# Optimization experiments

Measured on AMD Instinct MI355X. Metric: run time of the kernel, lower is better.

The kernel has to match this reference:

```python
import jax, jax.numpy as jnp
import numpy as np

NUM_SEQS = 4
SEQ_LEN = 2048
T = NUM_SEQS * SEQ_LEN          # total tokens
D_IN = 4096
D_OUT = 4096
NUM_ADAPTERS = 8
MAX_RANK = 64
CACHE_LEN = NUM_ADAPTERS * MAX_RANK  # 512 pages


def setup_inputs() -> dict:
    key = jax.random.key(0)
    ks = jax.random.split(key, 8)
    x = jax.random.normal(ks[0], (T, D_IN), dtype=jnp.float32)
    weight = jax.random.normal(ks[1], (D_OUT, D_IN), dtype=jnp.float32) * 0.02
    bias = jax.random.normal(ks[2], (D_OUT,), dtype=jnp.float32) * 0.02
    a_cache = jax.random.normal(ks[3], (CACHE_LEN, D_IN), dtype=jnp.float32) * 0.02
    b_cache = jax.random.normal(ks[4], (CACHE_LEN, D_OUT), dtype=jnp.float32) * 0.02
    b_start_loc = (jnp.arange(NUM_SEQS) * SEQ_LEN).astype(jnp.int32)
    b_adapter_ids = jax.random.randint(ks[5], (NUM_SEQS,), 0, NUM_ADAPTERS).astype(jnp.int32)
    b_scaling = jax.random.uniform(ks[6], (NUM_SEQS,), dtype=jnp.float32, minval=0.5, maxval=2.0)
    # page i for (adapter a, rank slot r) lives at a*MAX_RANK + r
    rank_page_table = jnp.arange(CACHE_LEN, dtype=jnp.int32).reshape(NUM_ADAPTERS, MAX_RANK)
    ranks = jax.random.randint(ks[7], (NUM_ADAPTERS,), 1, MAX_RANK + 1).astype(jnp.int32)
    return {"x": x, "weight": weight, "bias": bias, "a_cache": a_cache,
            "b_cache": b_cache, "b_start_loc": b_start_loc,
            "b_adapter_ids": b_adapter_ids, "b_scaling": b_scaling,
            "rank_page_table": rank_page_table, "ranks": ranks}


def reference(x, weight, bias, a_cache, b_cache, b_start_loc,
              b_adapter_ids, b_scaling, rank_page_table, ranks):
    t = x.shape[0]
    num_adapters, max_rank = rank_page_table.shape
    # map each token to its sequence -> adapter id / scaling (mbgmm dispatch)
    seg = jnp.searchsorted(b_start_loc, jnp.arange(t, dtype=b_start_loc.dtype),
                           side='right') - 1                      # [T]
    tok_adapter = b_adapter_ids[seg]                              # [T]
    tok_scale = b_scaling[seg]                                    # [T]
    # gather paged LoRA A/B weights per adapter: [A, R, D]
    A_all = a_cache[rank_page_table]                              # [A, R, D_in]
    B_all = b_cache[rank_page_table]                              # [A, R, D_out]
    # mbgmm_a: xa[t, r] = x[t] . A[adapter(t), r], zero beyond rank
    xa_all = jnp.einsum('td,ard->tar', x, A_all)                  # [T, A, R]
    rmask = (jnp.arange(max_rank)[None, :] < ranks[:, None])      # [A, R]
    onehot = (tok_adapter[:, None] == jnp.arange(num_adapters)[None, :])  # [T, A]
    sel = (onehot[:, :, None] & rmask[None, :, :]).astype(x.dtype)  # [T, A, R]
    xa_sel = xa_all * sel
    # mbgmm_b: lora_out[t] = scaling * sum_r xa[t, r] * B[adapter(t), r]
    lora_out = jnp.einsum('tar,aro->to', xa_sel, B_all) * tok_scale[:, None]
    base_out = x @ weight.T + bias
    return base_out + lora_out
```

## Files before the change

kernel.cpp:

```cpp
#include <hip/hip_runtime.h>
#include <hip/hip_bf16.h>

typedef unsigned short u16;
typedef unsigned int u32;
typedef __attribute__((ext_vector_type(8))) short bf16x8;
typedef __attribute__((ext_vector_type(4))) float f32x4;

#define T_TOK 8192
#define DIN 4096
#define DOUT 4096
#define N_SEQS 4
#define N_ADPT 8
#define MAXR 64
#define CACHE_LEN 512

__device__ __forceinline__ u16 f2bf(float f) {
    u32 u = __builtin_bit_cast(u32, f);
    u += 0x7fffu + ((u >> 16) & 1u);
    return (u16)(u >> 16);
}

__device__ __forceinline__ void load_lds16(const u16* g, u16* l) {
    __builtin_amdgcn_global_load_lds(
        (const __attribute__((address_space(1))) u32*)g,
        (__attribute__((address_space(3))) u32*)l, 16, 0, 0);
}

__global__ void cvt_kernel(const float* __restrict__ in, u16* __restrict__ out, int n4) {
    int i = blockIdx.x * blockDim.x + threadIdx.x;
    int stride = gridDim.x * blockDim.x;
    for (; i < n4; i += stride) {
        float4 v = reinterpret_cast<const float4*>(in)[i];
        ushort4 o;
        o.x = f2bf(v.x); o.y = f2bf(v.y); o.z = f2bf(v.z); o.w = f2bf(v.w);
        reinterpret_cast<ushort4*>(out)[i] = o;
    }
}

__global__ void build_bt(const float* __restrict__ b_cache, const int* __restrict__ rpt,
                         u16* __restrict__ Bt) {
    int id = blockIdx.x * 256 + threadIdx.x;
    int n  = id & (DOUT - 1);
    int rb = (id >> 12) & 7;
    int a  = id >> 15;
    union { u16 u[8]; uint4 v; } pack;
    #pragma unroll
    for (int j = 0; j < 8; ++j) {
        int r = rb * 8 + j;
        int page = rpt[a * MAXR + r];
        pack.u[j] = f2bf(b_cache[(long)page * DOUT + n]);
    }
    *reinterpret_cast<uint4*>(&Bt[((long)(a * DOUT + n)) * MAXR + rb * 8]) = pack.v;
}

__launch_bounds__(256)
__global__ void xa_kernel(const u16* __restrict__ xb, const u16* __restrict__ ab,
                          const int* __restrict__ b_start_loc,
                          const int* __restrict__ b_adapter_ids,
                          const float* __restrict__ b_scaling,
                          const int* __restrict__ rpt,
                          const int* __restrict__ ranks,
                          u16* __restrict__ xa) {
    int t0 = blockIdx.x * 128;
    int seg = 0;
    #pragma unroll
    for (int i = 1; i < N_SEQS; ++i) if (b_start_loc[i] <= t0) seg = i;
    int adapter = b_adapter_ids[seg];
    float scale = b_scaling[seg];
    int rank = ranks[adapter];

    __shared__ __attribute__((aligned(16))) u16 As[128 * 32];
    __shared__ __attribute__((aligned(16))) u16 Bs[64 * 32];

    int tid = threadIdx.x;
    int lane = tid & 63, wave = tid >> 6;
    int lr = lane & 15, lk = lane >> 4;

    int e0 = wave * 64 + lane;
    int e1 = 256 + e0;
    int ra0 = e0 >> 2, ca0 = (e0 & 3) * 8;
    int ra1 = e1 >> 2, ca1 = (e1 & 3) * 8;
    const u16* gA0 = xb + (long)(t0 + ra0) * DIN + ca0;
    const u16* gA1 = xb + (long)(t0 + ra1) * DIN + ca1;
    int rB = ra0;
    int page = rpt[adapter * MAXR + rB];
    const u16* gB = ab + (long)page * DIN + ca0;

    f32x4 acc[2][4] = {};

    for (int k0 = 0; k0 < DIN; k0 += 32) {
        load_lds16(gA0 + k0, As + wave * 512);
        load_lds16(gA1 + k0, As + 2048 + wave * 512);
        load_lds16(gB + k0,  Bs + wave * 512);
        asm volatile("s_waitcnt vmcnt(0)" ::: "memory");
        __syncthreads();
        bf16x8 af[2], bfr[4];
        #pragma unroll
        for (int m = 0; m < 2; ++m)
            af[m] = *(const bf16x8*)&As[(wave * 32 + m * 16 + lr) * 32 + lk * 8];
        #pragma unroll
        for (int n = 0; n < 4; ++n)
            bfr[n] = *(const bf16x8*)&Bs[(n * 16 + lr) * 32 + lk * 8];
        #pragma unroll
        for (int m = 0; m < 2; ++m)
            #pragma unroll
            for (int n = 0; n < 4; ++n)
                acc[m][n] = __builtin_amdgcn_mfma_f32_16x16x32_bf16(af[m], bfr[n], acc[m][n], 0, 0, 0);
        __syncthreads();
    }

    #pragma unroll
    for (int m = 0; m < 2; ++m) {
        int trow = t0 + wave * 32 + m * 16 + lk * 4;
        #pragma unroll
        for (int n = 0; n < 4; ++n) {
            int r = n * 16 + lr;
            #pragma unroll
            for (int j = 0; j < 4; ++j) {
                float v = (r < rank) ? acc[m][n][j] * scale : 0.0f;
                xa[(long)(trow + j) * MAXR + r] = f2bf(v);
            }
        }
    }
}

__launch_bounds__(512, 2)
__global__ void gemm256_kernel(const u16* __restrict__ xb, const u16* __restrict__ wb,
                               const float* __restrict__ bias,
                               const u16* __restrict__ xa, const u16* __restrict__ Bt,
                               const int* __restrict__ b_start_loc,
                               const int* __restrict__ b_adapter_ids,
                               float* __restrict__ out) {
    __shared__ __attribute__((aligned(16))) u16 lds[32768];

    int bid = blockIdx.x;
    int wgid = (bid & 7) * 64 + (bid >> 3);
    int mt = wgid >> 4, nt = wgid & 15;
    int brow = mt * 256, bcol = nt * 256;

    int seg = 0;
    #pragma unroll
    for (int i = 1; i < N_SEQS; ++i) if (b_start_loc[i] <= brow) seg = i;
    int adapter = b_adapter_ids[seg];

    int tid = threadIdx.x;
    int lane = tid & 63, wave = tid >> 6;
    int wm = wave >> 2, wn = wave & 3;
    int lr = lane & 15, lk = lane >> 4;

    int lsw = (tid & 7) ^ ((tid >> 3) & 7);
    int c8  = (lsw & 3) * 8;
    int r0  = (tid >> 3) * 2 + (lsw >> 2);
    const long odA0 = (long)(brow + r0) * DIN + c8;
    const long odA1 = odA0 + 128L * DIN;
    const long odB0 = (long)(bcol + r0) * DIN + c8;
    const long odB1 = odB0 + 128L * DIN;
    const long o6A0 = (long)(brow + r0) * MAXR + c8;
    const long o6A1 = o6A0 + 128L * MAXR;
    const long o6B0 = (long)(adapter * DOUT + bcol + r0) * MAXR + c8;
    const long o6B1 = o6B0 + 128L * MAXR;

    #define STAGE(T, buf)                                                          \
        do {                                                                       \
            u16* dA = lds + (buf) * 8192 + tid * 8;                                \
            u16* dB = lds + 16384 + (buf) * 8192 + tid * 8;                        \
            if ((T) < 128) {                                                       \
                long ko = (long)(T) * 32;                                          \
                load_lds16(xb + odA0 + ko, dA);                                    \
                load_lds16(xb + odA1 + ko, dA + 4096);                             \
                load_lds16(wb + odB0 + ko, dB);                                    \
                load_lds16(wb + odB1 + ko, dB + 4096);                             \
            } else {                                                               \
                long ko = (long)((T) - 128) * 32;                                  \
                load_lds16(xa + o6A0 + ko, dA);                                    \
                load_lds16(xa + o6A1 + ko, dA + 4096);                             \
                load_lds16(Bt + o6B0 + ko, dB);                                    \
                load_lds16(Bt + o6B1 + ko, dB + 4096);                             \
            }                                                                      \
        } while (0)

    const int laneByte = (lr >> 1) * 128 + 16 * ((((lr & 1) << 2) + lk) ^ (lr >> 1));
    const char* ldsc = (const char*)lds;
    const int cA = wm * 8192 + laneByte;
    const int cB = 32768 + wn * 4096 + laneByte;

    #define READF(FA, FB, par)                                                     \
        do {                                                                       \
            const char* pA = ldsc + (par) * 16384 + cA;                            \
            const char* pB = ldsc + (par) * 16384 + cB;                            \
            _Pragma("unroll")                                                      \
            for (int ni = 0; ni < 4; ++ni) FB[ni] = *(const bf16x8*)(pB + ni * 1024); \
            _Pragma("unroll")                                                      \
            for (int mi = 0; mi < 8; ++mi) FA[mi] = *(const bf16x8*)(pA + mi * 1024); \
        } while (0)

    #define MFMA32(FA, FB)                                                         \
        do {                                                                       \
            __builtin_amdgcn_s_setprio(1);                                         \
            _Pragma("unroll")                                                      \
            for (int mi = 0; mi < 8; ++mi)                                         \
                _Pragma("unroll")                                                  \
                for (int ni = 0; ni < 4; ++ni)                                     \
                    acc[mi][ni] = __builtin_amdgcn_mfma_f32_16x16x32_bf16(         \
                        FA[mi], FB[ni], acc[mi][ni], 0, 0, 0);                     \
            __builtin_amdgcn_s_setprio(0);                                         \
        } while (0)

    #define ENDBAR()                                                               \
        do {                                                                       \
            asm volatile("s_waitcnt lgkmcnt(0)" ::: "memory");                     \
            __builtin_amdgcn_sched_barrier(0);                                     \
            __builtin_amdgcn_s_barrier();                                          \
        } while (0)

    f32x4 acc[8][4] = {};
    bf16x8 fA0[8], fB0[4], fA1[8], fB1[4];

    STAGE(0, 0);
    STAGE(1, 1);
    asm volatile("s_waitcnt vmcnt(4)" ::: "memory");
    __builtin_amdgcn_s_barrier();
    READF(fA0, fB0, 0);
    ENDBAR();

    for (int t = 0; t < 130; t += 2) {
        STAGE((t + 2 < 130) ? t + 2 : 129, t & 1);
        asm volatile("s_waitcnt vmcnt(4)" ::: "memory");
        __builtin_amdgcn_s_barrier();
        READF(fA1, fB1, (t + 1) & 1);
        MFMA32(fA0, fB0);
        ENDBAR();

        STAGE((t + 3 < 130) ? t + 3 : 129, (t + 1) & 1);
        asm volatile("s_waitcnt vmcnt(4)" ::: "memory");
        __builtin_amdgcn_s_barrier();
        if (t + 2 < 130) READF(fA0, fB0, t & 1);
        MFMA32(fA1, fB1);
        ENDBAR();
    }
    asm volatile("s_waitcnt vmcnt(0)" ::: "memory");

    #undef STAGE
    #undef READF
    #undef MFMA32
    #undef ENDBAR

    #pragma unroll
    for (int m = 0; m < 8; ++m) {
        int orow = brow + wm * 128 + m * 16 + lk * 4;
        #pragma unroll
        for (int n = 0; n < 4; ++n) {
            int ocol = bcol + wn * 64 + n * 16 + lr;
            float bv = bias[ocol];
            #pragma unroll
            for (int j = 0; j < 4; ++j)
                out[(long)(orow + j) * DOUT + ocol] = acc[m][n][j] + bv;
        }
    }
}

extern "C" void kernel_launch(void* const* d_in, const int* in_sizes, int n_in,
                              void* d_out, int out_size, void* d_ws, size_t ws_size,
                              hipStream_t stream) {
    const float* x          = (const float*)d_in[0];
    const float* weight     = (const float*)d_in[1];
    const float* bias       = (const float*)d_in[2];
    const float* a_cache    = (const float*)d_in[3];
    const float* b_cache    = (const float*)d_in[4];
    const int*   b_start    = (const int*)d_in[5];
    const int*   b_adapter  = (const int*)d_in[6];
    const float* b_scaling  = (const float*)d_in[7];
    const int*   rpt        = (const int*)d_in[8];
    const int*   ranks      = (const int*)d_in[9];
    float* out = (float*)d_out;

    char* ws = (char*)d_ws;
    u16* xb = (u16*)ws; ws += (size_t)T_TOK * DIN * 2;
    u16* wb = (u16*)ws; ws += (size_t)DOUT * DIN * 2;
    u16* ab = (u16*)ws; ws += (size_t)CACHE_LEN * DIN * 2;
    u16* Bt = (u16*)ws; ws += (size_t)N_ADPT * DOUT * MAXR * 2;
    u16* xa = (u16*)ws; ws += (size_t)T_TOK * MAXR * 2;

    cvt_kernel<<<2048, 256, 0, stream>>>(x, xb, T_TOK * DIN / 4);
    cvt_kernel<<<2048, 256, 0, stream>>>(weight, wb, DOUT * DIN / 4);
    cvt_kernel<<<512, 256, 0, stream>>>(a_cache, ab, CACHE_LEN * DIN / 4);
    build_bt<<<(N_ADPT * 8 * DOUT) / 256, 256, 0, stream>>>(b_cache, rpt, Bt);
    xa_kernel<<<T_TOK / 128, 256, 0, stream>>>(xb, ab, b_start, b_adapter, b_scaling, rpt, ranks, xa);
    gemm256_kernel<<<(T_TOK / 256) * (DOUT / 256), 512, 0, stream>>>(xb, wb, bias, xa, Bt, b_start, b_adapter, out);
}
```

Baseline: 366.9 us.

## Use 32x32x16 MFMA in main GEMM and double-buffer xa kernel loads

The main GEMM now uses 32x32x16 bf16 MFMA instructions with a 4x2 grid of 16-wide accumulators instead of 8x4 16x16x32 tiles. The LDS fragment addressing and output-store indexing are rewritten to match the new operand layout. Fewer, larger MFMAs per k-step should raise matrix-core throughput and cut LDS reads per FLOP. Separately, the xa kernel gets double-buffered LDS with a prefetch of the next k-slice, overlapping global loads with compute. The risk is wrong swizzle or lane mapping and more register pressure.

```diff
diff --git a/kernel.cpp b/kernel.cpp
--- a/kernel.cpp
+++ b/kernel.cpp
@@ -5,6 +5,7 @@
 typedef unsigned int u32;
 typedef __attribute__((ext_vector_type(8))) short bf16x8;
 typedef __attribute__((ext_vector_type(4))) float f32x4;
+typedef __attribute__((ext_vector_type(16))) float f32x16;
 
 #define T_TOK 8192
 #define DIN 4096
@@ -69,8 +70,8 @@
     float scale = b_scaling[seg];
     int rank = ranks[adapter];
 
-    __shared__ __attribute__((aligned(16))) u16 As[128 * 32];
-    __shared__ __attribute__((aligned(16))) u16 Bs[64 * 32];
+    __shared__ __attribute__((aligned(16))) u16 As[2 * 4096];
+    __shared__ __attribute__((aligned(16))) u16 Bs[2 * 2048];
 
     int tid = threadIdx.x;
     int lane = tid & 63, wave = tid >> 6;
@@ -88,26 +89,42 @@
 
     f32x4 acc[2][4] = {};
 
-    for (int k0 = 0; k0 < DIN; k0 += 32) {
-        load_lds16(gA0 + k0, As + wave * 512);
-        load_lds16(gA1 + k0, As + 2048 + wave * 512);
-        load_lds16(gB + k0,  Bs + wave * 512);
-        asm volatile("s_waitcnt vmcnt(0)" ::: "memory");
-        __syncthreads();
+    #define XSTAGE(s, buf)                                                         \
+        do {                                                                       \
+            load_lds16(gA0 + (s) * 32, As + (buf) * 4096 + wave * 512);            \
+            load_lds16(gA1 + (s) * 32, As + (buf) * 4096 + 2048 + wave * 512);     \
+            load_lds16(gB + (s) * 32,  Bs + (buf) * 2048 + wave * 512);            \
+        } while (0)
+
+    XSTAGE(0, 0);
+    for (int s = 0; s < 128; ++s) {
+        int b = s & 1;
+        if (s < 127) {
+            XSTAGE(s + 1, b ^ 1);
+            asm volatile("s_waitcnt vmcnt(3)" ::: "memory");
+        } else {
+            asm volatile("s_waitcnt vmcnt(0)" ::: "memory");
+        }
+        __builtin_amdgcn_s_barrier();
+        __builtin_amdgcn_sched_barrier(0);
+
         bf16x8 af[2], bfr[4];
         #pragma unroll
         for (int m = 0; m < 2; ++m)
-            af[m] = *(const bf16x8*)&As[(wave * 32 + m * 16 + lr) * 32 + lk * 8];
+            af[m] = *(const bf16x8*)&As[b * 4096 + (wave * 32 + m * 16 + lr) * 32 + lk * 8];
         #pragma unroll
         for (int n = 0; n < 4; ++n)
-            bfr[n] = *(const bf16x8*)&Bs[(n * 16 + lr) * 32 + lk * 8];
+            bfr[n] = *(const bf16x8*)&Bs[b * 2048 + (n * 16 + lr) * 32 + lk * 8];
         #pragma unroll
         for (int m = 0; m < 2; ++m)
             #pragma unroll
             for (int n = 0; n < 4; ++n)
                 acc[m][n] = __builtin_amdgcn_mfma_f32_16x16x32_bf16(af[m], bfr[n], acc[m][n], 0, 0, 0);
-        __syncthreads();
-    }
+
+        __builtin_amdgcn_s_barrier();
+        __builtin_amdgcn_sched_barrier(0);
+    }
+    #undef XSTAGE
 
     #pragma unroll
     for (int m = 0; m < 2; ++m) {
@@ -146,7 +163,9 @@
     int tid = threadIdx.x;
     int lane = tid & 63, wave = tid >> 6;
     int wm = wave >> 2, wn = wave & 3;
+    int l5 = lane & 31, k8 = lane >> 5;
     int lr = lane & 15, lk = lane >> 4;
+    (void)lr; (void)lk;
 
     int lsw = (tid & 7) ^ ((tid >> 3) & 7);
     int c8  = (lsw & 3) * 8;
@@ -179,30 +198,38 @@
             }                                                                      \
         } while (0)
 
-    const int laneByte = (lr >> 1) * 128 + 16 * ((((lr & 1) << 2) + lk) ^ (lr >> 1));
+    const int lb0 = (l5 >> 1) * 128 + (((((l5 & 1) << 2) + 0 + k8) ^ ((l5 >> 1) & 7)) * 16);
+    const int lb1 = (l5 >> 1) * 128 + (((((l5 & 1) << 2) + 2 + k8) ^ ((l5 >> 1) & 7)) * 16);
     const char* ldsc = (const char*)lds;
-    const int cA = wm * 8192 + laneByte;
-    const int cB = 32768 + wn * 4096 + laneByte;
+    const int cA0 = wm * 8192 + lb0, cA1 = wm * 8192 + lb1;
+    const int cB0 = 32768 + wn * 4096 + lb0, cB1 = 32768 + wn * 4096 + lb1;
 
     #define READF(FA, FB, par)                                                     \
         do {                                                                       \
-            const char* pA = ldsc + (par) * 16384 + cA;                            \
-            const char* pB = ldsc + (par) * 16384 + cB;                            \
+            const char* pA0 = ldsc + (par) * 16384 + cA0;                          \
+            const char* pA1 = ldsc + (par) * 16384 + cA1;                          \
+            const char* pB0 = ldsc + (par) * 16384 + cB0;                          \
+            const char* pB1 = ldsc + (par) * 16384 + cB1;                          \
+            FB[0] = *(const bf16x8*)(pB0);        FB[1] = *(const bf16x8*)(pB0 + 2048); \
+            FB[2] = *(const bf16x8*)(pB1);        FB[3] = *(const bf16x8*)(pB1 + 2048); \
             _Pragma("unroll")                                                      \
-            for (int ni = 0; ni < 4; ++ni) FB[ni] = *(const bf16x8*)(pB + ni * 1024); \
-            _Pragma("unroll")                                                      \
-            for (int mi = 0; mi < 8; ++mi) FA[mi] = *(const bf16x8*)(pA + mi * 1024); \
-        } while (0)
-
-    #define MFMA32(FA, FB)                                                         \
+            for (int mi = 0; mi < 4; ++mi) {                                       \
+                FA[mi]     = *(const bf16x8*)(pA0 + mi * 2048);                    \
+                FA[4 + mi] = *(const bf16x8*)(pA1 + mi * 2048);                    \
+            }                                                                      \
+        } while (0)
+
+    #define MFMA16(FA, FB)                                                         \
         do {                                                                       \
             __builtin_amdgcn_s_setprio(1);                                         \
             _Pragma("unroll")                                                      \
-            for (int mi = 0; mi < 8; ++mi)                                         \
+            for (int ks = 0; ks < 2; ++ks)                                         \
                 _Pragma("unroll")                                                  \
-                for (int ni = 0; ni < 4; ++ni)                                     \
-                    acc[mi][ni] = __builtin_amdgcn_mfma_f32_16x16x32_bf16(         \
-                        FA[mi], FB[ni], acc[mi][ni], 0, 0, 0);                     \
+                for (int mi = 0; mi < 4; ++mi)                                     \
+                    _Pragma("unroll")                                              \
+                    for (int ni = 0; ni < 2; ++ni)                                 \
+                        acc[mi][ni] = __builtin_amdgcn_mfma_f32_32x32x16_bf16(     \
+                            FA[ks * 4 + mi], FB[ks * 2 + ni], acc[mi][ni], 0, 0, 0); \
             __builtin_amdgcn_s_setprio(0);                                         \
         } while (0)
 
@@ -213,7 +240,7 @@
             __builtin_amdgcn_s_barrier();                                          \
         } while (0)
 
-    f32x4 acc[8][4] = {};
+    f32x16 acc[4][2] = {};
     bf16x8 fA0[8], fB0[4], fA1[8], fB1[4];
 
     STAGE(0, 0);
@@ -228,33 +255,36 @@
         asm volatile("s_waitcnt vmcnt(4)" ::: "memory");
         __builtin_amdgcn_s_barrier();
         READF(fA1, fB1, (t + 1) & 1);
-        MFMA32(fA0, fB0);
+        MFMA16(fA0, fB0);
         ENDBAR();
 
         STAGE((t + 3 < 130) ? t + 3 : 129, (t + 1) & 1);
         asm volatile("s_waitcnt vmcnt(4)" ::: "memory");
         __builtin_amdgcn_s_barrier();
         if (t + 2 < 130) READF(fA0, fB0, t & 1);
-        MFMA32(fA1, fB1);
+        MFMA16(fA1, fB1);
         ENDBAR();
     }
     asm volatile("s_waitcnt vmcnt(0)" ::: "memory");
 
     #undef STAGE
     #undef READF
-    #undef MFMA32
+    #undef MFMA16
     #undef ENDBAR
 
     #pragma unroll
-    for (int m = 0; m < 8; ++m) {
-        int orow = brow + wm * 128 + m * 16 + lk * 4;
-        #pragma unroll
-        for (int n = 0; n < 4; ++n) {
-            int ocol = bcol + wn * 64 + n * 16 + lr;
+    for (int mi = 0; mi < 4; ++mi) {
+        #pragma unroll
+        for (int ni = 0; ni < 2; ++ni) {
+            int ocol = bcol + wn * 64 + ni * 32 + l5;
             float bv = bias[ocol];
             #pragma unroll
-            for (int j = 0; j < 4; ++j)
-                out[(long)(orow + j) * DOUT + ocol] = acc[m][n][j] + bv;
+            for (int g = 0; g < 4; ++g) {
+                int orow = brow + wm * 128 + mi * 32 + g * 8 + k8 * 4;
+                #pragma unroll
+                for (int j = 0; j < 4; ++j)
+                    out[(long)(orow + j) * DOUT + ocol] = acc[mi][ni][g * 4 + j] + bv;
+            }
         }
     }
 }
```

Result: slower. 389.2 us (+6.1%).

## Split-K the LoRA xa GEMM with double-buffered loads and merge convert kernels

Applied to the files above, without the earlier changes.

Merges the three fp32-to-bf16 conversion launches into a single kernel. Splits the xa (x·A) GEMM across four K segments so it launches 256 blocks instead of 64, and double-buffers its LDS loads so the next stage's copy overlaps the current MFMAs. A new xa_fin kernel sums the fp32 partials and applies rank masking and scaling. This targets under-occupancy and serialized load latency in the small xa kernel, at the cost of an extra launch and an 8 MB partial-sum buffer round trip.

```diff
diff --git a/kernel.cpp b/kernel.cpp
--- a/kernel.cpp
+++ b/kernel.cpp
@@ -26,14 +26,21 @@
         (__attribute__((address_space(3))) u32*)l, 16, 0, 0);
 }
 
-__global__ void cvt_kernel(const float* __restrict__ in, u16* __restrict__ out, int n4) {
-    int i = blockIdx.x * blockDim.x + threadIdx.x;
-    int stride = gridDim.x * blockDim.x;
-    for (; i < n4; i += stride) {
-        float4 v = reinterpret_cast<const float4*>(in)[i];
+__global__ void cvt_all(const float* __restrict__ x, const float* __restrict__ w,
+                        const float* __restrict__ a,
+                        u16* __restrict__ xb, u16* __restrict__ wb, u16* __restrict__ ab) {
+    const int n_x = T_TOK * DIN / 4, n_w = DOUT * DIN / 4, n_a = CACHE_LEN * DIN / 4;
+    int i = blockIdx.x * 256 + threadIdx.x;
+    int stride = gridDim.x * 256;
+    for (int j = i; j < n_x + n_w + n_a; j += stride) {
+        const float* src; u16* dst; int k;
+        if (j < n_x)            { src = x; dst = xb; k = j; }
+        else if (j < n_x + n_w) { src = w; dst = wb; k = j - n_x; }
+        else                    { src = a; dst = ab; k = j - n_x - n_w; }
+        float4 v = reinterpret_cast<const float4*>(src)[k];
         ushort4 o;
         o.x = f2bf(v.x); o.y = f2bf(v.y); o.z = f2bf(v.z); o.w = f2bf(v.w);
-        reinterpret_cast<ushort4*>(out)[i] = o;
+        reinterpret_cast<ushort4*>(dst)[k] = o;
     }
 }
 
@@ -57,20 +64,17 @@
 __global__ void xa_kernel(const u16* __restrict__ xb, const u16* __restrict__ ab,
                           const int* __restrict__ b_start_loc,
                           const int* __restrict__ b_adapter_ids,
-                          const float* __restrict__ b_scaling,
                           const int* __restrict__ rpt,
-                          const int* __restrict__ ranks,
-                          u16* __restrict__ xa) {
-    int t0 = blockIdx.x * 128;
+                          float* __restrict__ xa_part) {
+    int tblk = blockIdx.x >> 2, kseg = blockIdx.x & 3;
+    int t0 = tblk * 128;
     int seg = 0;
     #pragma unroll
     for (int i = 1; i < N_SEQS; ++i) if (b_start_loc[i] <= t0) seg = i;
     int adapter = b_adapter_ids[seg];
-    float scale = b_scaling[seg];
-    int rank = ranks[adapter];
-
-    __shared__ __attribute__((aligned(16))) u16 As[128 * 32];
-    __shared__ __attribute__((aligned(16))) u16 Bs[64 * 32];
+
+    __shared__ __attribute__((aligned(16))) u16 As[2 * 4096];
+    __shared__ __attribute__((aligned(16))) u16 Bs[2 * 2048];
 
     int tid = threadIdx.x;
     int lane = tid & 63, wave = tid >> 6;
@@ -80,35 +84,51 @@
     int e1 = 256 + e0;
     int ra0 = e0 >> 2, ca0 = (e0 & 3) * 8;
     int ra1 = e1 >> 2, ca1 = (e1 & 3) * 8;
-    const u16* gA0 = xb + (long)(t0 + ra0) * DIN + ca0;
-    const u16* gA1 = xb + (long)(t0 + ra1) * DIN + ca1;
-    int rB = ra0;
-    int page = rpt[adapter * MAXR + rB];
-    const u16* gB = ab + (long)page * DIN + ca0;
+    const u16* gA0 = xb + (long)(t0 + ra0) * DIN + kseg * 1024 + ca0;
+    const u16* gA1 = xb + (long)(t0 + ra1) * DIN + kseg * 1024 + ca1;
+    int page = rpt[adapter * MAXR + ra0];
+    const u16* gB = ab + (long)page * DIN + kseg * 1024 + ca0;
 
     f32x4 acc[2][4] = {};
 
-    for (int k0 = 0; k0 < DIN; k0 += 32) {
-        load_lds16(gA0 + k0, As + wave * 512);
-        load_lds16(gA1 + k0, As + 2048 + wave * 512);
-        load_lds16(gB + k0,  Bs + wave * 512);
-        asm volatile("s_waitcnt vmcnt(0)" ::: "memory");
-        __syncthreads();
+    #define XSTAGE(s, buf)                                                         \
+        do {                                                                       \
+            load_lds16(gA0 + (s) * 32, As + (buf) * 4096 + wave * 512);            \
+            load_lds16(gA1 + (s) * 32, As + (buf) * 4096 + 2048 + wave * 512);     \
+            load_lds16(gB + (s) * 32,  Bs + (buf) * 2048 + wave * 512);            \
+        } while (0)
+
+    XSTAGE(0, 0);
+    for (int s = 0; s < 32; ++s) {
+        int b = s & 1;
+        if (s < 31) {
+            XSTAGE(s + 1, b ^ 1);
+            asm volatile("s_waitcnt vmcnt(3)" ::: "memory");
+        } else {
+            asm volatile("s_waitcnt vmcnt(0)" ::: "memory");
+        }
+        __builtin_amdgcn_s_barrier();
+        __builtin_amdgcn_sched_barrier(0);
+
         bf16x8 af[2], bfr[4];
         #pragma unroll
         for (int m = 0; m < 2; ++m)
-            af[m] = *(const bf16x8*)&As[(wave * 32 + m * 16 + lr) * 32 + lk * 8];
+            af[m] = *(const bf16x8*)&As[b * 4096 + (wave * 32 + m * 16 + lr) * 32 + lk * 8];
         #pragma unroll
         for (int n = 0; n < 4; ++n)
-            bfr[n] = *(const bf16x8*)&Bs[(n * 16 + lr) * 32 + lk * 8];
+            bfr[n] = *(const bf16x8*)&Bs[b * 2048 + (n * 16 + lr) * 32 + lk * 8];
         #pragma unroll
         for (int m = 0; m < 2; ++m)
             #pragma unroll
             for (int n = 0; n < 4; ++n)
                 acc[m][n] = __builtin_amdgcn_mfma_f32_16x16x32_bf16(af[m], bfr[n], acc[m][n], 0, 0, 0);
-        __syncthreads();
-    }
-
+
+        __builtin_amdgcn_s_barrier();
+        __builtin_amdgcn_sched_barrier(0);
+    }
+    #undef XSTAGE
+
+    float* dst = xa_part + (long)kseg * T_TOK * MAXR;
     #pragma unroll
     for (int m = 0; m < 2; ++m) {
         int trow = t0 + wave * 32 + m * 16 + lk * 4;
@@ -116,12 +136,29 @@
         for (int n = 0; n < 4; ++n) {
             int r = n * 16 + lr;
             #pragma unroll
-            for (int j = 0; j < 4; ++j) {
-                float v = (r < rank) ? acc[m][n][j] * scale : 0.0f;
-                xa[(long)(trow + j) * MAXR + r] = f2bf(v);
-            }
+            for (int j = 0; j < 4; ++j)
+                dst[(long)(trow + j) * MAXR + r] = acc[m][n][j];
         }
     }
+}
+
+__global__ void xa_fin(const float* __restrict__ xa_part,
+                       const int* __restrict__ b_start_loc,
+                       const int* __restrict__ b_adapter_ids,
+                       const float* __restrict__ b_scaling,
+                       const int* __restrict__ ranks,
+                       u16* __restrict__ xa) {
+    const int N = T_TOK * MAXR;
+    int i = blockIdx.x * 256 + threadIdx.x;
+    if (i >= N) return;
+    int t = i >> 6, r = i & 63;
+    int seg = 0;
+    #pragma unroll
+    for (int s = 1; s < N_SEQS; ++s) if (b_start_loc[s] <= t) seg = s;
+    int adapter = b_adapter_ids[seg];
+    float v = xa_part[i] + xa_part[N + i] + xa_part[2 * N + i] + xa_part[3 * N + i];
+    v = (r < ranks[adapter]) ? v * b_scaling[seg] : 0.0f;
+    xa[i] = f2bf(v);
 }
 
 __launch_bounds__(512, 2)
@@ -275,16 +312,16 @@
     float* out = (float*)d_out;
 
     char* ws = (char*)d_ws;
-    u16* xb = (u16*)ws; ws += (size_t)T_TOK * DIN * 2;
-    u16* wb = (u16*)ws; ws += (size_t)DOUT * DIN * 2;
-    u16* ab = (u16*)ws; ws += (size_t)CACHE_LEN * DIN * 2;
-    u16* Bt = (u16*)ws; ws += (size_t)N_ADPT * DOUT * MAXR * 2;
-    u16* xa = (u16*)ws; ws += (size_t)T_TOK * MAXR * 2;
-
-    cvt_kernel<<<2048, 256, 0, stream>>>(x, xb, T_TOK * DIN / 4);
-    cvt_kernel<<<2048, 256, 0, stream>>>(weight, wb, DOUT * DIN / 4);
-    cvt_kernel<<<512, 256, 0, stream>>>(a_cache, ab, CACHE_LEN * DIN / 4);
+    u16*   xb      = (u16*)ws;   ws += (size_t)T_TOK * DIN * 2;
+    u16*   wb      = (u16*)ws;   ws += (size_t)DOUT * DIN * 2;
+    u16*   ab      = (u16*)ws;   ws += (size_t)CACHE_LEN * DIN * 2;
+    u16*   Bt      = (u16*)ws;   ws += (size_t)N_ADPT * DOUT * MAXR * 2;
+    u16*   xa      = (u16*)ws;   ws += (size_t)T_TOK * MAXR * 2;
+    float* xa_part = (float*)ws; ws += (size_t)4 * T_TOK * MAXR * 4;
+
+    cvt_all<<<2048, 256, 0, stream>>>(x, weight, a_cache, xb, wb, ab);
     build_bt<<<(N_ADPT * 8 * DOUT) / 256, 256, 0, stream>>>(b_cache, rpt, Bt);
-    xa_kernel<<<T_TOK / 128, 256, 0, stream>>>(xb, ab, b_start, b_adapter, b_scaling, rpt, ranks, xa);
+    xa_kernel<<<(T_TOK / 128) * 4, 256, 0, stream>>>(xb, ab, b_start, b_adapter, rpt, xa_part);
+    xa_fin<<<(T_TOK * MAXR + 255) / 256, 256, 0, stream>>>(xa_part, b_start, b_adapter, b_scaling, ranks, xa);
     gemm256_kernel<<<(T_TOK / 256) * (DOUT / 256), 512, 0, stream>>>(xb, wb, bias, xa, Bt, b_start, b_adapter, out);
 }
```

Measured after the change: 328.1 us. 1.12x faster.
